# Kernel optimization log

Measured on AMD Instinct MI355X. Metric: run time of the kernel, lower is better.

## Reference

```python
import jax, jax.numpy as jnp
import numpy as np

SCALE = 1.0 / 8.0  # source divides sim_M by literal 8 (== sqrt(d_k=64))


def setup_inputs() -> dict:
    key = jax.random.key(0)
    ks = jax.random.split(key, 7)
    B, S, D = 16, 2048, 512  # D = n_head * d_k = 8 * 64
    s = 1.0 / np.sqrt(D)
    return {
        "x": jax.random.normal(ks[0], (B, S, D), dtype=jnp.float32),
        "Wq": jax.random.normal(ks[1], (D, D), dtype=jnp.float32) * s,
        "bq": jax.random.normal(ks[2], (D,), dtype=jnp.float32) * 0.01,
        "Wk": jax.random.normal(ks[3], (D, D), dtype=jnp.float32) * s,
        "bk": jax.random.normal(ks[4], (D,), dtype=jnp.float32) * 0.01,
        "Wv": jax.random.normal(ks[5], (D, D), dtype=jnp.float32) * s,
        "bv": jax.random.normal(ks[6], (D,), dtype=jnp.float32) * 0.01,
    }


def reference(x, Wq, bq, Wk, bk, Wv, bv):
    # Manual QKV projections (no head split, matching the source code)
    q = jnp.einsum("bsd,de->bse", x, Wq) + bq  # [B,S,D]
    k = jnp.einsum("bsd,de->bse", x, Wk) + bk  # [B,S,D]
    v = jnp.einsum("bsd,de->bse", x, Wv) + bv  # [B,S,D]
    # bmm -> softmax -> bmm attention
    sim = jnp.einsum("bqe,bke->bqk", q, k) * SCALE  # [B,S,S]
    attn = jax.nn.softmax(sim, axis=-1)
    out = jnp.einsum("bqk,bkd->bqd", attn, v)  # [B,S,D]
    return out
```

## Files before the change

### kernel.cpp

```cpp
#include <hip/hip_runtime.h>
#include <math.h>

typedef _Float16 f16;
typedef _Float16 f16x8 __attribute__((ext_vector_type(8)));
typedef float f32x4 __attribute__((ext_vector_type(4)));

#define NB 16
#define SS 2048
#define DD 512

__device__ __forceinline__ void gl_lds16(const void* g, void* l) {
  __builtin_amdgcn_global_load_lds(
      (const __attribute__((address_space(1))) unsigned int*)g,
      (__attribute__((address_space(3))) unsigned int*)l, 16, 0, 0);
}

__global__ __launch_bounds__(256) void cast_kernel(const float* __restrict__ x,
                                                   f16* __restrict__ o) {
  size_t i = (size_t)blockIdx.x * 256 + threadIdx.x;
  const float4* p = (const float4*)x + i * 2;
  float4 a = p[0], b = p[1];
  f16x8 v = {(f16)a.x, (f16)a.y, (f16)a.z, (f16)a.w,
             (f16)b.x, (f16)b.y, (f16)b.z, (f16)b.w};
  *((f16x8*)o + i) = v;
}

__global__ __launch_bounds__(256) void transpose_kernel(const float* __restrict__ W,
                                                        f16* __restrict__ Wt) {
  __shared__ float t[32][33];
  int bx = blockIdx.x * 32, by = blockIdx.y * 32;
  int c = threadIdx.x & 31, r0 = threadIdx.x >> 5;
  for (int r = r0; r < 32; r += 8) t[r][c] = W[(size_t)(by + r) * DD + bx + c];
  __syncthreads();
  for (int r = r0; r < 32; r += 8) Wt[(size_t)(bx + r) * DD + by + c] = (f16)t[c][r];
}

__global__ __launch_bounds__(256) void gemm_kernel(
    const f16* __restrict__ A, long sAb, const f16* __restrict__ Bt, long sBb,
    f16* __restrict__ C, long sCb, int ldc, const float* __restrict__ bias,
    int bias_row, float scale) {
  A += (size_t)blockIdx.z * sAb;
  Bt += (size_t)blockIdx.z * sBb;
  C += (size_t)blockIdx.z * sCb;
  const int m0 = blockIdx.y * 128, n0 = blockIdx.x * 128;
  __shared__ f16 Ash[128 * 32];
  __shared__ f16 Bsh[128 * 32];
  const int tid = threadIdx.x, lane = tid & 63, wave = tid >> 6;
  const int wm = wave & 1, wn = wave >> 1;
  const int l15 = lane & 15, lq = lane >> 4;
  f32x4 acc[4][4] = {};
  const int srow = tid >> 2, part = tid & 3;
  const f16* gA = A + (size_t)(m0 + srow) * DD + part * 8;
  const f16* gB = Bt + (size_t)(n0 + srow) * DD + part * 8;
  f16* lA = &Ash[tid * 8];
  f16* lB = &Bsh[tid * 8];
  for (int kt = 0; kt < 16; ++kt) {
    gl_lds16(gA + kt * 32, lA);
    gl_lds16(gA + 64 * DD + kt * 32, lA + 2048);
    gl_lds16(gB + kt * 32, lB);
    gl_lds16(gB + 64 * DD + kt * 32, lB + 2048);
    __syncthreads();
    f16x8 af[4], bf[4];
#pragma unroll
    for (int i = 0; i < 4; ++i)
      af[i] = *(const f16x8*)&Ash[(64 * wm + 16 * i + l15) * 32 + lq * 8];
#pragma unroll
    for (int j = 0; j < 4; ++j)
      bf[j] = *(const f16x8*)&Bsh[(64 * wn + 16 * j + l15) * 32 + lq * 8];
#pragma unroll
    for (int i = 0; i < 4; ++i)
#pragma unroll
      for (int j = 0; j < 4; ++j)
        acc[i][j] = __builtin_amdgcn_mfma_f32_16x16x32_f16(af[i], bf[j], acc[i][j], 0, 0, 0);
    __syncthreads();
  }
#pragma unroll
  for (int i = 0; i < 4; ++i) {
    int rb = 64 * wm + 16 * i + lq * 4;
#pragma unroll
    for (int j = 0; j < 4; ++j) {
      int cc = n0 + 64 * wn + 16 * j + l15;
#pragma unroll
      for (int r = 0; r < 4; ++r) {
        int rr = m0 + rb + r;
        float bv = bias_row ? bias[rr] : bias[cc];
        C[(size_t)rr * ldc + cc] = (f16)((acc[i][j][r] + bv) * scale);
      }
    }
  }
}

__global__ __launch_bounds__(512, 2) void attn_kernel(
    const f16* __restrict__ Q, const f16* __restrict__ K,
    const f16* __restrict__ Vt, float* __restrict__ out) {
  const int id = blockIdx.x;
  const int b = (id & 7) + ((id >> 7) << 3);
  const int qt = (id >> 3) & 15;
  const int tid = threadIdx.x, lane = tid & 63, wave = tid >> 6;
  const int l15 = lane & 15, lq = lane >> 4;

  __shared__ __align__(16) f16 Kl[2][32][520];
  __shared__ __align__(16) f16 Vl[2][512][32];
  __shared__ __align__(16) f16 Psh[128][40];

  const f16* qp = Q + ((size_t)(b * SS + qt * 128 + wave * 16 + l15)) * DD + lq * 8;
  f16x8 qf[16];
#pragma unroll
  for (int kk = 0; kk < 16; ++kk) qf[kk] = *(const f16x8*)(qp + kk * 32);

  const f16* Kb = K + (size_t)b * SS * DD;
  const f16* Vb = Vt + (size_t)b * DD * SS;

  const int sdata = (lane & 3) ^ ((lane >> 3) & 3);
  const int vrow = lane >> 2;
  const int vs_off = (lq ^ ((l15 >> 1) & 3)) * 8;

  f16x8 onef;
#pragma unroll
  for (int j = 0; j < 8; ++j) onef[j] = (f16)1.0f;

  auto stage = [&](int sb, int kb) {
#pragma unroll
    for (int rr = 0; rr < 4; ++rr) {
      int row = wave * 4 + rr;
      gl_lds16(Kb + ((size_t)(kb + row)) * DD + lane * 8, &Kl[sb][row][lane * 8]);
    }
#pragma unroll
    for (int i = 0; i < 4; ++i) {
      int e0 = wave * 64 + i * 16;
      gl_lds16(Vb + (size_t)(e0 + vrow) * SS + kb + sdata * 8,
               (f16*)&Vl[sb][e0][0] + lane * 8);
    }
  };

  stage(0, 0);
  __syncthreads();

  f32x4 acco[32] = {};
  f32x4 accl = {};
  float m_i[4] = {-1e30f, -1e30f, -1e30f, -1e30f};

  for (int it = 0; it < 64; ++it) {
    const int buf = it & 1;
    if (it < 63) stage(buf ^ 1, (it + 1) * 32);
    f32x4 sa0 = {}, sa1 = {};
#pragma unroll
    for (int kk = 0; kk < 16; ++kk) {
      f16x8 b0 = *(const f16x8*)&Kl[buf][l15][kk * 32 + lq * 8];
      f16x8 b1 = *(const f16x8*)&Kl[buf][16 + l15][kk * 32 + lq * 8];
      sa0 = __builtin_amdgcn_mfma_f32_16x16x32_f16(qf[kk], b0, sa0, 0, 0, 0);
      sa1 = __builtin_amdgcn_mfma_f32_16x16x32_f16(qf[kk], b1, sa1, 0, 0, 0);
    }
    float mx[4];
#pragma unroll
    for (int r = 0; r < 4; ++r) mx[r] = fmaxf(sa0[r], sa1[r]);
#pragma unroll
    for (int d = 1; d < 16; d <<= 1)
#pragma unroll
      for (int r = 0; r < 4; ++r) mx[r] = fmaxf(mx[r], __shfl_xor(mx[r], d));
    bool need = false;
#pragma unroll
    for (int r = 0; r < 4; ++r) need |= (mx[r] > m_i[r] + 8.0f);
    if (__any(need)) {
      float al[4];
#pragma unroll
      for (int r = 0; r < 4; ++r) {
        float mn = fmaxf(m_i[r], mx[r]);
        al[r] = __expf(m_i[r] - mn);
        m_i[r] = mn;
      }
#pragma unroll
      for (int t = 0; t < 32; ++t)
#pragma unroll
        for (int r = 0; r < 4; ++r) acco[t][r] *= al[r];
#pragma unroll
      for (int r = 0; r < 4; ++r) accl[r] *= al[r];
    }
#pragma unroll
    for (int r = 0; r < 4; ++r) {
      Psh[16 * wave + 4 * lq + r][l15] = (f16)__expf(sa0[r] - m_i[r]);
      Psh[16 * wave + 4 * lq + r][16 + l15] = (f16)__expf(sa1[r] - m_i[r]);
    }
    f16x8 pa = *(const f16x8*)&Psh[16 * wave + l15][lq * 8];
    accl = __builtin_amdgcn_mfma_f32_16x16x32_f16(pa, onef, accl, 0, 0, 0);
#pragma unroll
    for (int nn = 0; nn < 32; ++nn) {
      f16x8 vf = *(const f16x8*)&Vl[buf][nn * 16 + l15][vs_off];
      acco[nn] = __builtin_amdgcn_mfma_f32_16x16x32_f16(pa, vf, acco[nn], 0, 0, 0);
    }
    __syncthreads();
  }
  float inv[4];
#pragma unroll
  for (int r = 0; r < 4; ++r) inv[r] = 1.0f / accl[r];
  const size_t ob = ((size_t)(b * SS + qt * 128 + wave * 16 + 4 * lq)) * DD + l15;
#pragma unroll
  for (int nn = 0; nn < 32; ++nn)
#pragma unroll
    for (int r = 0; r < 4; ++r)
      out[ob + (size_t)r * DD + nn * 16] = acco[nn][r] * inv[r];
}

extern "C" void kernel_launch(void* const* d_in, const int* in_sizes, int n_in,
                              void* d_out, int out_size, void* d_ws, size_t ws_size,
                              hipStream_t stream) {
  const float* x = (const float*)d_in[0];
  const float* Wq = (const float*)d_in[1];
  const float* bq = (const float*)d_in[2];
  const float* Wk = (const float*)d_in[3];
  const float* bk = (const float*)d_in[4];
  const float* Wv = (const float*)d_in[5];
  const float* bv = (const float*)d_in[6];
  float* out = (float*)d_out;
  f16* ws = (f16*)d_ws;
  const size_t NX = (size_t)NB * SS * DD;
  f16* xh = ws;
  f16* Qh = ws + NX;
  f16* Kh = ws + 2 * NX;
  f16* Vth = ws + 3 * NX;
  f16* WqT = ws + 4 * NX;
  f16* WkT = WqT + DD * DD;
  f16* WvT = WkT + DD * DD;

  cast_kernel<<<NX / 8 / 256, 256, 0, stream>>>(x, xh);
  dim3 tg(16, 16);
  transpose_kernel<<<tg, 256, 0, stream>>>(Wq, WqT);
  transpose_kernel<<<tg, 256, 0, stream>>>(Wk, WkT);
  transpose_kernel<<<tg, 256, 0, stream>>>(Wv, WvT);
  gemm_kernel<<<dim3(4, 256, 1), 256, 0, stream>>>(xh, 0, WqT, 0, Qh, 0, DD, bq, 0, 0.125f);
  gemm_kernel<<<dim3(4, 256, 1), 256, 0, stream>>>(xh, 0, WkT, 0, Kh, 0, DD, bk, 0, 1.0f);
  gemm_kernel<<<dim3(16, 4, NB), 256, 0, stream>>>(WvT, 0, xh, (long)SS * DD, Vth,
                                                   (long)DD * SS, SS, bv, 1, 1.0f);
  attn_kernel<<<256, 512, 0, stream>>>(Qh, Kh, Vth, out);
}
```

Before: 421.5 us.

## Transpose QK^T MFMA and exchange P fragments via lane shuffles instead of LDS

Swaps the MFMA operand order so each lane holds scores for a single query row. The row max then needs only two cross-lane shuffles, and the running max becomes one scalar per lane. The probability tile is packed to f16 pairs and redistributed into the PV A-operand layout with shuffles and selects, which removes the Psh shared-memory round trip. In exchange it adds per-row shuffles for the rescale factors and more select logic, and the register-level permutation is intricate and could be wrong.

```diff
diff --git a/kernel.cpp b/kernel.cpp
--- a/kernel.cpp
+++ b/kernel.cpp
@@ -2,6 +2,7 @@
 #include <math.h>
 
 typedef _Float16 f16;
+typedef _Float16 f16x2 __attribute__((ext_vector_type(2)));
 typedef _Float16 f16x8 __attribute__((ext_vector_type(8)));
 typedef float f32x4 __attribute__((ext_vector_type(4)));
 
@@ -13,6 +14,11 @@
   __builtin_amdgcn_global_load_lds(
       (const __attribute__((address_space(1))) unsigned int*)g,
       (__attribute__((address_space(3))) unsigned int*)l, 16, 0, 0);
+}
+
+__device__ __forceinline__ int pk2(float a, float b) {
+  f16x2 t = {(f16)a, (f16)b};
+  return __builtin_bit_cast(int, t);
 }
 
 __global__ __launch_bounds__(256) void cast_kernel(const float* __restrict__ x,
@@ -101,7 +107,6 @@
 
   __shared__ __align__(16) f16 Kl[2][32][520];
   __shared__ __align__(16) f16 Vl[2][512][32];
-  __shared__ __align__(16) f16 Psh[128][40];
 
   const f16* qp = Q + ((size_t)(b * SS + qt * 128 + wave * 16 + l15)) * DD + lq * 8;
   f16x8 qf[16];
@@ -138,7 +143,7 @@
 
   f32x4 acco[32] = {};
   f32x4 accl = {};
-  float m_i[4] = {-1e30f, -1e30f, -1e30f, -1e30f};
+  float m = -1e30f;
 
   for (int it = 0; it < 64; ++it) {
     const int buf = it & 1;
@@ -148,40 +153,45 @@
     for (int kk = 0; kk < 16; ++kk) {
       f16x8 b0 = *(const f16x8*)&Kl[buf][l15][kk * 32 + lq * 8];
       f16x8 b1 = *(const f16x8*)&Kl[buf][16 + l15][kk * 32 + lq * 8];
-      sa0 = __builtin_amdgcn_mfma_f32_16x16x32_f16(qf[kk], b0, sa0, 0, 0, 0);
-      sa1 = __builtin_amdgcn_mfma_f32_16x16x32_f16(qf[kk], b1, sa1, 0, 0, 0);
-    }
-    float mx[4];
-#pragma unroll
-    for (int r = 0; r < 4; ++r) mx[r] = fmaxf(sa0[r], sa1[r]);
-#pragma unroll
-    for (int d = 1; d < 16; d <<= 1)
-#pragma unroll
-      for (int r = 0; r < 4; ++r) mx[r] = fmaxf(mx[r], __shfl_xor(mx[r], d));
-    bool need = false;
-#pragma unroll
-    for (int r = 0; r < 4; ++r) need |= (mx[r] > m_i[r] + 8.0f);
-    if (__any(need)) {
-      float al[4];
-#pragma unroll
-      for (int r = 0; r < 4; ++r) {
-        float mn = fmaxf(m_i[r], mx[r]);
-        al[r] = __expf(m_i[r] - mn);
-        m_i[r] = mn;
-      }
+      sa0 = __builtin_amdgcn_mfma_f32_16x16x32_f16(b0, qf[kk], sa0, 0, 0, 0);
+      sa1 = __builtin_amdgcn_mfma_f32_16x16x32_f16(b1, qf[kk], sa1, 0, 0, 0);
+    }
+    float lm = fmaxf(fmaxf(fmaxf(sa0[0], sa0[1]), fmaxf(sa0[2], sa0[3])),
+                     fmaxf(fmaxf(sa1[0], sa1[1]), fmaxf(sa1[2], sa1[3])));
+    if (__any(lm > m + 8.0f)) {
+      float mx = lm;
+      mx = fmaxf(mx, __shfl_xor(mx, 16));
+      mx = fmaxf(mx, __shfl_xor(mx, 32));
+      float mn = fmaxf(m, mx);
+      float al = __expf(m - mn);
+      m = mn;
+      float alr[4];
+#pragma unroll
+      for (int r = 0; r < 4; ++r) alr[r] = __shfl(al, 4 * lq + r);
 #pragma unroll
       for (int t = 0; t < 32; ++t)
 #pragma unroll
-        for (int r = 0; r < 4; ++r) acco[t][r] *= al[r];
-#pragma unroll
-      for (int r = 0; r < 4; ++r) accl[r] *= al[r];
-    }
-#pragma unroll
-    for (int r = 0; r < 4; ++r) {
-      Psh[16 * wave + 4 * lq + r][l15] = (f16)__expf(sa0[r] - m_i[r]);
-      Psh[16 * wave + 4 * lq + r][16 + l15] = (f16)__expf(sa1[r] - m_i[r]);
-    }
-    f16x8 pa = *(const f16x8*)&Psh[16 * wave + l15][lq * 8];
+        for (int r = 0; r < 4; ++r) acco[t][r] *= alr[r];
+#pragma unroll
+      for (int r = 0; r < 4; ++r) accl[r] *= alr[r];
+    }
+    int A0 = pk2(__expf(sa0[0] - m), __expf(sa0[1] - m));
+    int A1 = pk2(__expf(sa0[2] - m), __expf(sa0[3] - m));
+    int B0 = pk2(__expf(sa1[0] - m), __expf(sa1[1] - m));
+    int B1 = pk2(__expf(sa1[2] - m), __expf(sa1[3] - m));
+    const bool low = (lq < 2);
+    int s0 = low ? B0 : A0, s1 = low ? B1 : A1;
+    int X0 = __shfl_xor(s0, 32), X1 = __shfl_xor(s1, 32);
+    int Y0 = low ? A0 : B0, Y1 = low ? A1 : B1;
+    const bool sx = (lq == 0) || (lq == 3);
+    int t0 = sx ? X0 : Y0, t1 = sx ? X1 : Y1;
+    int Z0 = __shfl_xor(t0, 16), Z1 = __shfl_xor(t1, 16);
+    union PU { int i[4]; f16x8 v; } pu;
+    pu.i[0] = (lq == 0) ? Y0 : ((lq == 2) ? X0 : Z0);
+    pu.i[1] = (lq == 0) ? Y1 : ((lq == 2) ? X1 : Z1);
+    pu.i[2] = (lq == 1) ? X0 : ((lq == 3) ? Y0 : Z0);
+    pu.i[3] = (lq == 1) ? X1 : ((lq == 3) ? Y1 : Z1);
+    f16x8 pa = pu.v;
     accl = __builtin_amdgcn_mfma_f32_16x16x32_f16(pa, onef, accl, 0, 0, 0);
 #pragma unroll
     for (int nn = 0; nn < 32; ++nn) {
```

Result: faster. 392.7 us (-6.9%).
